# Optimization experiments

Measured on AMD Instinct MI355X. Metric: run time of the kernel, lower is better.

Reference implementation:

```python
import jax, jax.numpy as jnp
import numpy as np

N_MID = 100000
D = 64
B = 64
S = 256
K = 10
BIG_NEG = -2.0**32 + 1.0


def _din(q, facts, mask, W1, b1, W2, b2, W3, b3):
    # q broadcastable to facts shape; facts [..., T, D]; mask [..., T]
    qb = jnp.broadcast_to(q, facts.shape)
    x = jnp.concatenate([qb, facts, qb - facts, qb * facts], axis=-1)  # [..., T, 4D]
    h = jax.nn.sigmoid(x @ W1 + b1)
    h = jax.nn.sigmoid(h @ W2 + b2)
    s = (h @ W3 + b3)[..., 0]  # [..., T]
    s = jnp.where(mask == 1.0, s, BIG_NEG)
    a = jax.nn.softmax(s, axis=-1)
    return jnp.einsum('...t,...td->...d', a, facts)


def _prelu(x, alpha):
    return jnp.maximum(x, 0.0) + alpha * jnp.minimum(x, 0.0)


def setup_inputs():
    key = jax.random.key(0)
    ks = iter(jax.random.split(key, 48))
    def nrm(shape, scale=0.05):
        return jax.random.normal(next(ks), shape, dtype=jnp.float32) * scale
    inp = {}
    inp['mid'] = jax.random.randint(next(ks), (B,), 0, N_MID)
    inp['click_his'] = jax.random.randint(next(ks), (B, S), 0, N_MID)
    inp['unclick_his'] = jax.random.randint(next(ks), (B, K * S), 0, N_MID)
    inp['click_mask'] = jnp.ones((B, S), jnp.float32)
    inp['unclick_mask'] = jnp.ones((B, K * S), jnp.float32)
    inp['emb'] = nrm((N_MID, D), 0.1)
    for p in ('s', 'c', 'u'):  # search / click / unclick attention MLPs
        inp[p + 'W1'] = nrm((4 * D, 80)); inp[p + 'b1'] = jnp.zeros((80,), jnp.float32)
        inp[p + 'W2'] = nrm((80, 40));    inp[p + 'b2'] = jnp.zeros((40,), jnp.float32)
        inp[p + 'W3'] = nrm((40, 1));     inp[p + 'b3'] = jnp.zeros((1,), jnp.float32)
    F = 3 * D
    inp['bn_g'] = jnp.ones((F,), jnp.float32); inp['bn_b'] = jnp.zeros((F,), jnp.float32)
    inp['bn_m'] = jnp.zeros((F,), jnp.float32); inp['bn_v'] = jnp.ones((F,), jnp.float32)
    inp['fW1'] = nrm((F, 200)); inp['fb1'] = jnp.zeros((200,), jnp.float32); inp['a1'] = 0.25 * jnp.ones((200,), jnp.float32)
    inp['fW2'] = nrm((200, 80)); inp['fb2'] = jnp.zeros((80,), jnp.float32); inp['a2'] = 0.25 * jnp.ones((80,), jnp.float32)
    inp['fW3'] = nrm((80, 2)); inp['fb3'] = jnp.zeros((2,), jnp.float32)
    return inp


def reference(mid, click_his, unclick_his, click_mask, unclick_mask, emb,
              sW1, sb1, sW2, sb2, sW3, sb3,
              cW1, cb1, cW2, cb2, cW3, cb3,
              uW1, ub1, uW2, ub2, uW3, ub3,
              bn_g, bn_b, bn_m, bn_v,
              fW1, fb1, a1, fW2, fb2, a2, fW3, fb3):
    item = emb[mid]                                        # [B, D]
    click = emb[click_his] * click_mask[..., None]         # [B, S, D]
    unclick = emb[unclick_his] * unclick_mask[..., None]   # [B, K*S, D]
    uf = unclick.reshape(B, S, K, D)
    umask = unclick_mask.reshape(B, S, K)
    # din_attention_1: per clicked item, attend over its K unclicked items
    un_att = _din(click[:, :, None, :], uf, umask, sW1, sb1, sW2, sb2, sW3, sb3)  # [B, S, D]
    # denoise: project unclick rep onto click rep (shared component)
    dot = jnp.sum(un_att * click, axis=-1, keepdims=True)
    nrm2 = jnp.sum(click * click, axis=-1, keepdims=True) + 1e-12  # ||target||^2
    shared = dot * click / nrm2
    att1 = _din(item[:, None, :], click + shared, click_mask, cW1, cb1, cW2, cb2, cW3, cb3)  # [B, D]
    att2 = _din(item[:, None, :], un_att, click_mask, uW1, ub1, uW2, ub2, uW3, ub3)          # [B, D]
    x = jnp.concatenate([item, att1, att2], axis=-1)  # [B, 3D]
    x = (x - bn_m) / jnp.sqrt(bn_v + 1e-3) * bn_g + bn_b  # inference batchnorm
    x = _prelu(x @ fW1 + fb1, a1)
    x = _prelu(x @ fW2 + fb2, a2)
    logits = x @ fW3 + fb3
    return jax.nn.softmax(logits, axis=-1) + 1e-8
```

## Files before the change

kernel.cpp:

```cpp
#include <hip/hip_runtime.h>
#include <hip/hip_bf16.h>
#include <math.h>

#define BB 64
#define SS 256
#define KK 10
#define DD 64
#define FF 192
#define FH1 200
#define FH2 80
#define BIG_NEG_F (-4294967295.0f)

#define XSTR 200
#define H1STR 104

#define W1ELTS (80 * XSTR)
#define W2ELTS (48 * H1STR)
#define WREG   (W1ELTS + W2ELTS)

typedef __bf16 bfrag __attribute__((ext_vector_type(8)));
typedef float f32x4 __attribute__((ext_vector_type(4)));

__device__ __forceinline__ float sigm_(float x) { return 1.0f / (1.0f + __expf(-x)); }

__global__ __launch_bounds__(256) void k_prep(
    const float* __restrict__ sW1, const float* __restrict__ sW2,
    const float* __restrict__ cW1, const float* __restrict__ cW2,
    const float* __restrict__ uW1, const float* __restrict__ uW2,
    __bf16* __restrict__ Wt)
{
    const int p = blockIdx.x, g = blockIdx.y;
    const float* W1 = (p == 0) ? sW1 : (p == 1) ? cW1 : uW1;
    const float* W2 = (p == 0) ? sW2 : (p == 1) ? cW2 : uW2;
    __bf16* o1 = Wt + p * WREG;
    __bf16* o2 = o1 + W1ELTS;
    for (int e = g * 256 + threadIdx.x; e < W1ELTS; e += 2560) {
        const int n = e / XSTR, k = e % XSTR;
        float v = 0.0f;
        if (k < 64)       v = W1[k * 80 + n] + W1[(128 + k) * 80 + n];
        else if (k < 128) { const int kk = k - 64;  v = W1[(64 + kk) * 80 + n] - W1[(128 + kk) * 80 + n]; }
        else if (k < 192) { const int kk = k - 128; v = W1[(192 + kk) * 80 + n]; }
        o1[e] = (__bf16)v;
    }
    for (int e = g * 256 + threadIdx.x; e < W2ELTS; e += 2560) {
        const int n = e / H1STR, k = e % H1STR;
        o2[e] = (__bf16)((n < 40 && k < 80) ? W2[k * 40 + n] : 0.0f);
    }
}

__device__ __forceinline__ void mlp_core(
    const float* qv, const float* fv,
    const __bf16* __restrict__ sW1, __bf16* __restrict__ sH1w,
    const bfrag* wb2, const float* b1v, const float* b2v, const float* w3v,
    int quad, int l15, float* score)
{
    bfrag af[6];
    #pragma unroll
    for (int j = 0; j < 8; ++j) {
        af[0][j] = (__bf16)qv[j];
        af[1][j] = (__bf16)qv[8 + j];
        af[2][j] = (__bf16)fv[j];
        af[3][j] = (__bf16)fv[8 + j];
        af[4][j] = (__bf16)(qv[j] * fv[j]);
        af[5][j] = (__bf16)(qv[8 + j] * fv[8 + j]);
    }

    f32x4 acc[5];
    #pragma unroll
    for (int nt = 0; nt < 5; ++nt) acc[nt] = (f32x4){0.f, 0.f, 0.f, 0.f};
    {
        const __bf16* wbase = sW1 + l15 * XSTR + quad * 8;
        #pragma unroll
        for (int nt = 0; nt < 5; ++nt) {
            const __bf16* wp = wbase + nt * 16 * XSTR;
            #pragma unroll
            for (int kc = 0; kc < 6; ++kc)
                acc[nt] = __builtin_amdgcn_mfma_f32_16x16x32_bf16(
                    af[kc], *(const bfrag*)(wp + kc * 32), acc[nt], 0, 0, 0);
        }
    }

    #pragma unroll
    for (int nt = 0; nt < 5; ++nt) {
        #pragma unroll
        for (int rg = 0; rg < 4; ++rg)
            sH1w[(quad * 4 + rg) * H1STR + nt * 16 + l15] =
                (__bf16)sigm_(acc[nt][rg] + b1v[nt]);
    }
    #pragma unroll
    for (int rg = 0; rg < 4; ++rg)
        sH1w[(quad * 4 + rg) * H1STR + 80 + l15] = (__bf16)0.0f;

    bfrag af2[3];
    {
        const __bf16* hrow = sH1w + l15 * H1STR + quad * 8;
        #pragma unroll
        for (int kc = 0; kc < 3; ++kc) af2[kc] = *(const bfrag*)(hrow + kc * 32);
    }
    f32x4 acc2[3];
    #pragma unroll
    for (int nt = 0; nt < 3; ++nt) acc2[nt] = (f32x4){0.f, 0.f, 0.f, 0.f};
    #pragma unroll
    for (int nt = 0; nt < 3; ++nt)
        #pragma unroll
        for (int kc = 0; kc < 3; ++kc)
            acc2[nt] = __builtin_amdgcn_mfma_f32_16x16x32_bf16(
                af2[kc], wb2[nt * 3 + kc], acc2[nt], 0, 0, 0);

    float part[4] = {0.f, 0.f, 0.f, 0.f};
    #pragma unroll
    for (int nt = 0; nt < 3; ++nt) {
        #pragma unroll
        for (int rg = 0; rg < 4; ++rg)
            part[rg] += sigm_(acc2[nt][rg] + b2v[nt]) * w3v[nt];
    }
    #pragma unroll
    for (int off = 1; off < 16; off <<= 1) {
        #pragma unroll
        for (int rg = 0; rg < 4; ++rg)
            part[rg] += __shfl_xor(part[rg], off, 64);
    }
    #pragma unroll
    for (int rg = 0; rg < 4; ++rg) score[rg] = part[rg];
}

__global__ __launch_bounds__(320) void k_din0(
    const int* __restrict__ click_his, const int* __restrict__ unclick_his,
    const float* __restrict__ click_mask, const float* __restrict__ unclick_mask,
    const float* __restrict__ emb, const __bf16* __restrict__ Wt,
    const float* __restrict__ b1, const float* __restrict__ b2,
    const float* __restrict__ W3, const float* __restrict__ b3,
    float* __restrict__ unatt, float* __restrict__ coef)
{
    __shared__ __align__(16) __bf16 sW1[80 * XSTR];
    __shared__ __align__(16) __bf16 sH1[5 * 16 * H1STR];
    __shared__ float ssc[80];

    const int t = threadIdx.x;
    const int wave = t >> 6, lane = t & 63;
    const int quad = lane >> 4, l15 = lane & 15;

    {
        const uint4* s1 = (const uint4*)Wt;
        uint4* d1 = (uint4*)sW1;
        for (int e = t; e < W1ELTS / 8; e += 320) d1[e] = s1[e];
    }

    bfrag wb2[9];
    float b1v[5], b2v[3], w3v[3];
    {
        const __bf16* w2g = Wt + W1ELTS;
        #pragma unroll
        for (int nt = 0; nt < 3; ++nt)
            #pragma unroll
            for (int kc = 0; kc < 3; ++kc)
                wb2[nt * 3 + kc] = *(const bfrag*)(w2g + (nt * 16 + l15) * H1STR + kc * 32 + quad * 8);
        #pragma unroll
        for (int nt = 0; nt < 5; ++nt) b1v[nt] = b1[nt * 16 + l15];
        #pragma unroll
        for (int nt = 0; nt < 3; ++nt) {
            const int n = nt * 16 + l15;
            b2v[nt] = (n < 40) ? b2[n] : 0.0f;
            w3v[nt] = (n < 40) ? W3[n] : 0.0f;
        }
    }
    const float b3v = b3[0];

    const int row = 16 * wave + l15;
    const int m   = blockIdx.x * 80 + row;
    const int bs  = blockIdx.x * 8 + row / 10;
    float qv[16], fv[16];
    {
        const float* qp = emb + (size_t)click_his[bs] * DD;
        const float* fp = emb + (size_t)unclick_his[m] * DD;
        const float qs = click_mask[bs], fs = unclick_mask[m];
        const int c = quad * 8;
        *(float4*)(qv + 0)  = *(const float4*)(qp + c);
        *(float4*)(qv + 4)  = *(const float4*)(qp + c + 4);
        *(float4*)(qv + 8)  = *(const float4*)(qp + 32 + c);
        *(float4*)(qv + 12) = *(const float4*)(qp + 32 + c + 4);
        *(float4*)(fv + 0)  = *(const float4*)(fp + c);
        *(float4*)(fv + 4)  = *(const float4*)(fp + c + 4);
        *(float4*)(fv + 8)  = *(const float4*)(fp + 32 + c);
        *(float4*)(fv + 12) = *(const float4*)(fp + 32 + c + 4);
        #pragma unroll
        for (int i = 0; i < 16; ++i) { qv[i] *= qs; fv[i] *= fs; }
    }

    float fpre[2][KK], qpre[2];
    #pragma unroll
    for (int jj = 0; jj < 2; ++jj) {
        const int j = wave + 5 * jj;
        if (j < 8) {
            const int bsj = blockIdx.x * 8 + j;
            #pragma unroll
            for (int k = 0; k < KK; ++k) {
                const int off = bsj * KK + k;
                fpre[jj][k] = emb[(size_t)unclick_his[off] * DD + lane] * unclick_mask[off];
            }
            qpre[jj] = emb[(size_t)click_his[bsj] * DD + lane] * click_mask[bsj];
        }
    }
    __syncthreads();

    float score[4];
    mlp_core(qv, fv, sW1, sH1 + wave * 16 * H1STR, wb2, b1v, b2v, w3v, quad, l15, score);

    if (l15 == 0) {
        #pragma unroll
        for (int rg = 0; rg < 4; ++rg) {
            const int r2 = 16 * wave + quad * 4 + rg;
            const int m2 = blockIdx.x * 80 + r2;
            ssc[r2] = (unclick_mask[m2] == 1.0f) ? (score[rg] + b3v) : BIG_NEG_F;
        }
    }
    __syncthreads();

    #pragma unroll
    for (int jj = 0; jj < 2; ++jj) {
        const int j = wave + 5 * jj;
        if (j >= 8) continue;
        const int bsj = blockIdx.x * 8 + j;
        float a[KK];
        float mx = -INFINITY;
        #pragma unroll
        for (int k = 0; k < KK; ++k) { a[k] = ssc[j * KK + k]; mx = fmaxf(mx, a[k]); }
        float sum = 0.0f;
        #pragma unroll
        for (int k = 0; k < KK; ++k) { a[k] = __expf(a[k] - mx); sum += a[k]; }
        const float inv = 1.0f / sum;
        float acc3 = 0.0f;
        #pragma unroll
        for (int k = 0; k < KK; ++k) acc3 += a[k] * fpre[jj][k];
        acc3 *= inv;
        unatt[(size_t)bsj * DD + lane] = acc3;
        const float qv2 = qpre[jj];
        float dp = acc3 * qv2, nq = qv2 * qv2;
        #pragma unroll
        for (int o = 32; o > 0; o >>= 1) {
            dp += __shfl_down(dp, o, 64);
            nq += __shfl_down(nq, o, 64);
        }
        if (lane == 0) coef[bsj] = 1.0f + dp / (nq + 1e-12f);
    }
}

__global__ __launch_bounds__(128) void k_din12(
    const int* __restrict__ mid, const int* __restrict__ click_his,
    const float* __restrict__ click_mask,
    const float* __restrict__ emb, const float* __restrict__ unatt,
    const float* __restrict__ coef, const __bf16* __restrict__ Wt,
    const float* __restrict__ cb1, const float* __restrict__ cb2,
    const float* __restrict__ cW3, const float* __restrict__ cb3,
    const float* __restrict__ ub1, const float* __restrict__ ub2,
    const float* __restrict__ uW3, const float* __restrict__ ub3,
    float* __restrict__ scores_c, float* __restrict__ scores_u)
{
    __shared__ __align__(16) __bf16 sW1[80 * XSTR];
    __shared__ __align__(16) __bf16 sH1[2 * 16 * H1STR];

    const int t = threadIdx.x;
    const int mode = blockIdx.y;
    const int wave = t >> 6, lane = t & 63;
    const int quad = lane >> 4, l15 = lane & 15;

    const float* b1 = mode ? ub1 : cb1;
    const float* b2 = mode ? ub2 : cb2;
    const float* W3 = mode ? uW3 : cW3;
    const float* b3 = mode ? ub3 : cb3;
    const __bf16* wreg = Wt + (mode + 1) * WREG;

    {
        const uint4* s1 = (const uint4*)wreg;
        uint4* d1 = (uint4*)sW1;
        for (int e = t; e < W1ELTS / 8; e += 128) d1[e] = s1[e];
    }

    bfrag wb2[9];
    float b1v[5], b2v[3], w3v[3];
    {
        const __bf16* w2g = wreg + W1ELTS;
        #pragma unroll
        for (int nt = 0; nt < 3; ++nt)
            #pragma unroll
            for (int kc = 0; kc < 3; ++kc)
                wb2[nt * 3 + kc] = *(const bfrag*)(w2g + (nt * 16 + l15) * H1STR + kc * 32 + quad * 8);
        #pragma unroll
        for (int nt = 0; nt < 5; ++nt) b1v[nt] = b1[nt * 16 + l15];
        #pragma unroll
        for (int nt = 0; nt < 3; ++nt) {
            const int n = nt * 16 + l15;
            b2v[nt] = (n < 40) ? b2[n] : 0.0f;
            w3v[nt] = (n < 40) ? W3[n] : 0.0f;
        }
    }
    const float b3v = b3[0];

    const int row = 16 * wave + l15;
    const int m   = blockIdx.x * 32 + row;
    const int b   = m >> 8;
    float qv[16], fv[16];
    {
        const float* qp = emb + (size_t)mid[b] * DD;
        const float* fp; float fs;
        if (mode == 0) { fp = emb + (size_t)click_his[m] * DD; fs = click_mask[m] * coef[m]; }
        else           { fp = unatt + (size_t)m * DD; fs = 1.0f; }
        const int c = quad * 8;
        *(float4*)(qv + 0)  = *(const float4*)(qp + c);
        *(float4*)(qv + 4)  = *(const float4*)(qp + c + 4);
        *(float4*)(qv + 8)  = *(const float4*)(qp + 32 + c);
        *(float4*)(qv + 12) = *(const float4*)(qp + 32 + c + 4);
        *(float4*)(fv + 0)  = *(const float4*)(fp + c);
        *(float4*)(fv + 4)  = *(const float4*)(fp + c + 4);
        *(float4*)(fv + 8)  = *(const float4*)(fp + 32 + c);
        *(float4*)(fv + 12) = *(const float4*)(fp + 32 + c + 4);
        #pragma unroll
        for (int i = 0; i < 16; ++i) fv[i] *= fs;
    }
    __syncthreads();

    float score[4];
    mlp_core(qv, fv, sW1, sH1 + wave * 16 * H1STR, wb2, b1v, b2v, w3v, quad, l15, score);

    if (l15 == 0) {
        float* dst = mode ? scores_u : scores_c;
        #pragma unroll
        for (int rg = 0; rg < 4; ++rg) {
            const int m2 = blockIdx.x * 32 + 16 * wave + quad * 4 + rg;
            dst[m2] = (click_mask[m2] == 1.0f) ? (score[rg] + b3v) : BIG_NEG_F;
        }
    }
}

__global__ __launch_bounds__(1024) void k_tail(
    const int* __restrict__ mid, const int* __restrict__ click_his,
    const float* __restrict__ click_mask,
    const float* __restrict__ emb, const float* __restrict__ unatt,
    const float* __restrict__ coef,
    const float* __restrict__ scores_c, const float* __restrict__ scores_u,
    const float* __restrict__ bn_g, const float* __restrict__ bn_b,
    const float* __restrict__ bn_m, const float* __restrict__ bn_v,
    const float* __restrict__ fW1, const float* __restrict__ fb1, const float* __restrict__ a1,
    const float* __restrict__ fW2, const float* __restrict__ fb2, const float* __restrict__ a2,
    const float* __restrict__ fW3, const float* __restrict__ fb3,
    float* __restrict__ out)
{
    const int b = blockIdx.x, t = threadIdx.x;
    const int wave = t >> 6, lane = t & 63;
    const int ty = wave >> 3, w8 = wave & 7;
    const int s0 = w8 * 32;

    __shared__ float sa[2][SS];
    __shared__ float smax[16], ssum[16];
    __shared__ float part[16][72];
    __shared__ float x[FF];
    __shared__ float ph1[4][FH1];
    __shared__ float h1s[FH1];
    __shared__ float ph2[8][FH2];
    __shared__ float h2s[FH2];
    __shared__ float red2[2];

    if (t < DD) x[t] = emb[(size_t)mid[b] * DD + t];

    const float* scp = ty ? scores_u : scores_c;
    const float sc = (lane < 32) ? scp[b * SS + s0 + lane] : -INFINITY;
    float mloc = sc;
    #pragma unroll
    for (int o = 32; o > 0; o >>= 1) mloc = fmaxf(mloc, __shfl_xor(mloc, o, 64));
    if (lane == 0) smax[wave] = mloc;
    __syncthreads();

    float mt = smax[ty * 8];
    #pragma unroll
    for (int i = 1; i < 8; ++i) mt = fmaxf(mt, smax[ty * 8 + i]);
    const float e = (lane < 32) ? __expf(sc - mt) : 0.0f;
    if (lane < 32) sa[ty][s0 + lane] = e;
    float sloc = e;
    #pragma unroll
    for (int o = 32; o > 0; o >>= 1) sloc += __shfl_xor(sloc, o, 64);
    if (lane == 0) ssum[wave] = sloc;
    __syncthreads();

    float den = 0.0f;
    #pragma unroll
    for (int i = 0; i < 8; ++i) den += ssum[ty * 8 + i];
    const float inv = 1.0f / den;

    float acc = 0.0f;
    #pragma unroll 8
    for (int i = 0; i < 32; ++i) {
        const int s2 = s0 + i;
        const int bs = b * SS + s2;
        const float fv = ty ? unatt[(size_t)bs * DD + lane]
                            : emb[(size_t)click_his[bs] * DD + lane] * click_mask[bs] * coef[bs];
        acc += sa[ty][s2] * fv;
    }
    part[wave][lane] = acc * inv;
    __syncthreads();

    if (t < 128) {
        const int tt = t >> 6, d = t & 63;
        float v = 0.0f;
        #pragma unroll
        for (int i = 0; i < 8; ++i) v += part[tt * 8 + i][d];
        x[DD + tt * DD + d] = v;
    }
    __syncthreads();

    if (t < FF) x[t] = (x[t] - bn_m[t]) * rsqrtf(bn_v[t] + 1e-3f) * bn_g[t] + bn_b[t];
    __syncthreads();

    if (t < 800) {
        const int n = t % FH1, c = t / FH1;
        float p = 0.0f;
        #pragma unroll 8
        for (int i = c * 48; i < c * 48 + 48; ++i) p += x[i] * fW1[i * FH1 + n];
        ph1[c][n] = p;
    }
    __syncthreads();
    if (t < FH1) {
        const float a = ph1[0][t] + ph1[1][t] + ph1[2][t] + ph1[3][t] + fb1[t];
        h1s[t] = fmaxf(a, 0.0f) + a1[t] * fminf(a, 0.0f);
    }
    __syncthreads();

    if (t < 640) {
        const int n = t % FH2, c = t / FH2;
        float p = 0.0f;
        #pragma unroll 5
        for (int i = c * 25; i < c * 25 + 25; ++i) p += h1s[i] * fW2[i * FH2 + n];
        ph2[c][n] = p;
    }
    __syncthreads();
    if (t < FH2) {
        float a = fb2[t];
        #pragma unroll
        for (int c = 0; c < 8; ++c) a += ph2[c][t];
        h2s[t] = fmaxf(a, 0.0f) + a2[t] * fminf(a, 0.0f);
    }
    __syncthreads();

    if (t < 128) {
        const int o = t >> 6;
        float p = h2s[lane] * fW3[lane * 2 + o];
        if (lane < 16) p += h2s[64 + lane] * fW3[(64 + lane) * 2 + o];
        #pragma unroll
        for (int off = 32; off > 0; off >>= 1) p += __shfl_down(p, off, 64);
        if (lane == 0) red2[o] = p + fb3[o];
    }
    __syncthreads();
    if (t == 0) {
        const float l0 = red2[0], l1 = red2[1];
        const float mx = fmaxf(l0, l1);
        const float e0 = __expf(l0 - mx), e1 = __expf(l1 - mx);
        const float invs = 1.0f / (e0 + e1);
        out[b * 2 + 0] = e0 * invs + 1e-8f;
        out[b * 2 + 1] = e1 * invs + 1e-8f;
    }
}

extern "C" void kernel_launch(void* const* d_in, const int* in_sizes, int n_in,
                              void* d_out, int out_size, void* d_ws, size_t ws_size,
                              hipStream_t stream) {
    const int*   mid          = (const int*)d_in[0];
    const int*   click_his    = (const int*)d_in[1];
    const int*   unclick_his  = (const int*)d_in[2];
    const float* click_mask   = (const float*)d_in[3];
    const float* unclick_mask = (const float*)d_in[4];
    const float* emb          = (const float*)d_in[5];
    const float* sW1 = (const float*)d_in[6];  const float* sb1 = (const float*)d_in[7];
    const float* sW2 = (const float*)d_in[8];  const float* sb2 = (const float*)d_in[9];
    const float* sW3 = (const float*)d_in[10]; const float* sb3 = (const float*)d_in[11];
    const float* cW1 = (const float*)d_in[12]; const float* cb1 = (const float*)d_in[13];
    const float* cW2 = (const float*)d_in[14]; const float* cb2 = (const float*)d_in[15];
    const float* cW3 = (const float*)d_in[16]; const float* cb3 = (const float*)d_in[17];
    const float* uW1 = (const float*)d_in[18]; const float* ub1 = (const float*)d_in[19];
    const float* uW2 = (const float*)d_in[20]; const float* ub2 = (const float*)d_in[21];
    const float* uW3 = (const float*)d_in[22]; const float* ub3 = (const float*)d_in[23];
    const float* bn_g = (const float*)d_in[24]; const float* bn_b = (const float*)d_in[25];
    const float* bn_m = (const float*)d_in[26]; const float* bn_v = (const float*)d_in[27];
    const float* fW1 = (const float*)d_in[28]; const float* fb1 = (const float*)d_in[29];
    const float* a1  = (const float*)d_in[30];
    const float* fW2 = (const float*)d_in[31]; const float* fb2 = (const float*)d_in[32];
    const float* a2  = (const float*)d_in[33];
    const float* fW3 = (const float*)d_in[34]; const float* fb3 = (const float*)d_in[35];

    float* out = (float*)d_out;

    char* w = (char*)d_ws;
    __bf16* Wt      = (__bf16*)(w + 0);
    float* scores_c = (float*)(w + 125952);
    float* scores_u = (float*)(w + 191488);
    float* coef     = (float*)(w + 257024);
    float* unatt    = (float*)(w + 322560);

    hipLaunchKernelGGL(k_prep, dim3(3, 10), dim3(256), 0, stream,
        sW1, sW2, cW1, cW2, uW1, uW2, Wt);

    hipLaunchKernelGGL(k_din0, dim3(2048), dim3(320), 0, stream,
        click_his, unclick_his, click_mask, unclick_mask, emb, Wt,
        sb1, sb2, sW3, sb3, unatt, coef);

    hipLaunchKernelGGL(k_din12, dim3(512, 2), dim3(128), 0, stream,
        mid, click_his, click_mask, emb, unatt, coef, Wt,
        cb1, cb2, cW3, cb3, ub1, ub2, uW3, ub3, scores_c, scores_u);

    hipLaunchKernelGGL(k_tail, dim3(BB), dim3(1024), 0, stream,
        mid, click_his, click_mask, emb, unatt, coef, scores_c, scores_u,
        bn_g, bn_b, bn_m, bn_v, fW1, fb1, a1, fW2, fb2, a2, fW3, fb3, out);
}
```

Measured before the change: 246.1 us.

## Amortize shared weight staging over more rows per block with prefetched gathers

k_din0 now gives each wave 80 rows (5 MFMA tiles, 8 click items) and loops over them, prefetching the next tile's embedding gathers while the current tile runs the MLP. Blocks drop from 2048 to 512, so the 32KB W1 copy into LDS is paid a quarter as often. k_din12 doubles rows per block to amortize the same staging, and k_prep now reads W1 coalesced while writing transposed. The cost is fewer blocks in flight and more registers for the double-buffered row data, which may reduce parallelism for the latency-bound gathers.

```diff
diff --git a/kernel.cpp b/kernel.cpp
--- a/kernel.cpp
+++ b/kernel.cpp
@@ -34,13 +34,14 @@
     const float* W2 = (p == 0) ? sW2 : (p == 1) ? cW2 : uW2;
     __bf16* o1 = Wt + p * WREG;
     __bf16* o2 = o1 + W1ELTS;
-    for (int e = g * 256 + threadIdx.x; e < W1ELTS; e += 2560) {
-        const int n = e / XSTR, k = e % XSTR;
-        float v = 0.0f;
-        if (k < 64)       v = W1[k * 80 + n] + W1[(128 + k) * 80 + n];
-        else if (k < 128) { const int kk = k - 64;  v = W1[(64 + kk) * 80 + n] - W1[(128 + kk) * 80 + n]; }
-        else if (k < 192) { const int kk = k - 128; v = W1[(192 + kk) * 80 + n]; }
-        o1[e] = (__bf16)v;
+    for (int e = g * 256 + threadIdx.x; e < 200 * 80; e += 2560) {
+        const int k = e / 80, n = e % 80;
+        float v;
+        if (k < 64)       v = W1[k * 80 + n] + W1[(k + 128) * 80 + n];
+        else if (k < 128) v = W1[k * 80 + n] - W1[(k + 64) * 80 + n];
+        else if (k < 192) v = W1[(k + 64) * 80 + n];
+        else              v = 0.0f;
+        o1[n * XSTR + k] = (__bf16)v;
     }
     for (int e = g * 256 + threadIdx.x; e < W2ELTS; e += 2560) {
         const int n = e / H1STR, k = e % H1STR;
@@ -124,7 +125,7 @@
     for (int rg = 0; rg < 4; ++rg) score[rg] = part[rg];
 }
 
-__global__ __launch_bounds__(320) void k_din0(
+__global__ __launch_bounds__(256) void k_din0(
     const int* __restrict__ click_his, const int* __restrict__ unclick_his,
     const float* __restrict__ click_mask, const float* __restrict__ unclick_mask,
     const float* __restrict__ emb, const __bf16* __restrict__ Wt,
@@ -133,8 +134,8 @@
     float* __restrict__ unatt, float* __restrict__ coef)
 {
     __shared__ __align__(16) __bf16 sW1[80 * XSTR];
-    __shared__ __align__(16) __bf16 sH1[5 * 16 * H1STR];
-    __shared__ float ssc[80];
+    __shared__ __align__(16) __bf16 sH1[4][16 * H1STR];
+    __shared__ float ssc[4][80];
 
     const int t = threadIdx.x;
     const int wave = t >> 6, lane = t & 63;
@@ -143,7 +144,7 @@
     {
         const uint4* s1 = (const uint4*)Wt;
         uint4* d1 = (uint4*)sW1;
-        for (int e = t; e < W1ELTS / 8; e += 320) d1[e] = s1[e];
+        for (int e = t; e < W1ELTS / 8; e += 256) d1[e] = s1[e];
     }
 
     bfrag wb2[9];
@@ -166,15 +167,15 @@
     }
     const float b3v = b3[0];
 
-    const int row = 16 * wave + l15;
-    const int m   = blockIdx.x * 80 + row;
-    const int bs  = blockIdx.x * 8 + row / 10;
-    float qv[16], fv[16];
-    {
+    const int wbase = (blockIdx.x * 4 + wave) * 80;
+    const int c = quad * 8;
+
+    auto gload = [&](int tt, float* qv, float* fv) {
+        const int m  = wbase + tt * 16 + l15;
+        const int bs = m / 10;
         const float* qp = emb + (size_t)click_his[bs] * DD;
         const float* fp = emb + (size_t)unclick_his[m] * DD;
         const float qs = click_mask[bs], fs = unclick_mask[m];
-        const int c = quad * 8;
         *(float4*)(qv + 0)  = *(const float4*)(qp + c);
         *(float4*)(qv + 4)  = *(const float4*)(qp + c + 4);
         *(float4*)(qv + 8)  = *(const float4*)(qp + 32 + c);
@@ -185,56 +186,56 @@
         *(float4*)(fv + 12) = *(const float4*)(fp + 32 + c + 4);
         #pragma unroll
         for (int i = 0; i < 16; ++i) { qv[i] *= qs; fv[i] *= fs; }
-    }
-
-    float fpre[2][KK], qpre[2];
-    #pragma unroll
-    for (int jj = 0; jj < 2; ++jj) {
-        const int j = wave + 5 * jj;
-        if (j < 8) {
-            const int bsj = blockIdx.x * 8 + j;
+    };
+
+    float qv[2][16], fv[2][16];
+    gload(0, qv[0], fv[0]);
+    __syncthreads();
+
+    for (int tt = 0; tt < 5; ++tt) {
+        if (tt < 4) gload(tt + 1, qv[(tt + 1) & 1], fv[(tt + 1) & 1]);
+        float score[4];
+        mlp_core(qv[tt & 1], fv[tt & 1], sW1, sH1[wave], wb2, b1v, b2v, w3v, quad, l15, score);
+        if (l15 == 0) {
             #pragma unroll
-            for (int k = 0; k < KK; ++k) {
-                const int off = bsj * KK + k;
-                fpre[jj][k] = emb[(size_t)unclick_his[off] * DD + lane] * unclick_mask[off];
+            for (int rg = 0; rg < 4; ++rg) {
+                const int r2 = tt * 16 + quad * 4 + rg;
+                const int m2 = wbase + r2;
+                ssc[wave][r2] = (unclick_mask[m2] == 1.0f) ? (score[rg] + b3v) : BIG_NEG_F;
             }
-            qpre[jj] = emb[(size_t)click_his[bsj] * DD + lane] * click_mask[bsj];
-        }
-    }
-    __syncthreads();
-
-    float score[4];
-    mlp_core(qv, fv, sW1, sH1 + wave * 16 * H1STR, wb2, b1v, b2v, w3v, quad, l15, score);
-
-    if (l15 == 0) {
-        #pragma unroll
-        for (int rg = 0; rg < 4; ++rg) {
-            const int r2 = 16 * wave + quad * 4 + rg;
-            const int m2 = blockIdx.x * 80 + r2;
-            ssc[r2] = (unclick_mask[m2] == 1.0f) ? (score[rg] + b3v) : BIG_NEG_F;
-        }
-    }
-    __syncthreads();
-
-    #pragma unroll
-    for (int jj = 0; jj < 2; ++jj) {
-        const int j = wave + 5 * jj;
-        if (j >= 8) continue;
-        const int bsj = blockIdx.x * 8 + j;
+        }
+    }
+    __syncthreads();
+
+    float fr[2][KK], qr[2];
+    auto kload = [&](int j) {
+        const int bsj = blockIdx.x * 32 + wave * 8 + j;
+        const int jj = j & 1;
+        #pragma unroll
+        for (int k = 0; k < KK; ++k) {
+            const int off = bsj * KK + k;
+            fr[jj][k] = emb[(size_t)unclick_his[off] * DD + lane] * unclick_mask[off];
+        }
+        qr[jj] = emb[(size_t)click_his[bsj] * DD + lane] * click_mask[bsj];
+    };
+    kload(0);
+    for (int j = 0; j < 8; ++j) {
+        if (j < 7) kload(j + 1);
+        const int bsj = blockIdx.x * 32 + wave * 8 + j;
         float a[KK];
         float mx = -INFINITY;
         #pragma unroll
-        for (int k = 0; k < KK; ++k) { a[k] = ssc[j * KK + k]; mx = fmaxf(mx, a[k]); }
+        for (int k = 0; k < KK; ++k) { a[k] = ssc[wave][j * KK + k]; mx = fmaxf(mx, a[k]); }
         float sum = 0.0f;
         #pragma unroll
         for (int k = 0; k < KK; ++k) { a[k] = __expf(a[k] - mx); sum += a[k]; }
         const float inv = 1.0f / sum;
         float acc3 = 0.0f;
         #pragma unroll
-        for (int k = 0; k < KK; ++k) acc3 += a[k] * fpre[jj][k];
+        for (int k = 0; k < KK; ++k) acc3 += a[k] * fr[j & 1][k];
         acc3 *= inv;
         unatt[(size_t)bsj * DD + lane] = acc3;
-        const float qv2 = qpre[jj];
+        const float qv2 = qr[j & 1];
         float dp = acc3 * qv2, nq = qv2 * qv2;
         #pragma unroll
         for (int o = 32; o > 0; o >>= 1) {
@@ -245,7 +246,7 @@
     }
 }
 
-__global__ __launch_bounds__(128) void k_din12(
+__global__ __launch_bounds__(256) void k_din12(
     const int* __restrict__ mid, const int* __restrict__ click_his,
     const float* __restrict__ click_mask,
     const float* __restrict__ emb, const float* __restrict__ unatt,
@@ -257,7 +258,7 @@
     float* __restrict__ scores_c, float* __restrict__ scores_u)
 {
     __shared__ __align__(16) __bf16 sW1[80 * XSTR];
-    __shared__ __align__(16) __bf16 sH1[2 * 16 * H1STR];
+    __shared__ __align__(16) __bf16 sH1[4][16 * H1STR];
 
     const int t = threadIdx.x;
     const int mode = blockIdx.y;
@@ -273,7 +274,7 @@
     {
         const uint4* s1 = (const uint4*)wreg;
         uint4* d1 = (uint4*)sW1;
-        for (int e = t; e < W1ELTS / 8; e += 128) d1[e] = s1[e];
+        for (int e = t; e < W1ELTS / 8; e += 256) d1[e] = s1[e];
     }
 
     bfrag wb2[9];
@@ -297,7 +298,7 @@
     const float b3v = b3[0];
 
     const int row = 16 * wave + l15;
-    const int m   = blockIdx.x * 32 + row;
+    const int m   = blockIdx.x * 64 + row;
     const int b   = m >> 8;
     float qv[16], fv[16];
     {
@@ -320,13 +321,13 @@
     __syncthreads();
 
     float score[4];
-    mlp_core(qv, fv, sW1, sH1 + wave * 16 * H1STR, wb2, b1v, b2v, w3v, quad, l15, score);
+    mlp_core(qv, fv, sW1, sH1[wave], wb2, b1v, b2v, w3v, quad, l15, score);
 
     if (l15 == 0) {
         float* dst = mode ? scores_u : scores_c;
         #pragma unroll
         for (int rg = 0; rg < 4; ++rg) {
-            const int m2 = blockIdx.x * 32 + 16 * wave + quad * 4 + rg;
+            const int m2 = blockIdx.x * 64 + 16 * wave + quad * 4 + rg;
             dst[m2] = (click_mask[m2] == 1.0f) ? (score[rg] + b3v) : BIG_NEG_F;
         }
     }
@@ -411,11 +412,11 @@
     __syncthreads();
 
     if (t < 800) {
-        const int n = t % FH1, c = t / FH1;
+        const int n = t % FH1, cc = t / FH1;
         float p = 0.0f;
         #pragma unroll 8
-        for (int i = c * 48; i < c * 48 + 48; ++i) p += x[i] * fW1[i * FH1 + n];
-        ph1[c][n] = p;
+        for (int i = cc * 48; i < cc * 48 + 48; ++i) p += x[i] * fW1[i * FH1 + n];
+        ph1[cc][n] = p;
     }
     __syncthreads();
     if (t < FH1) {
@@ -425,17 +426,17 @@
     __syncthreads();
 
     if (t < 640) {
-        const int n = t % FH2, c = t / FH2;
+        const int n = t % FH2, cc = t / FH2;
         float p = 0.0f;
         #pragma unroll 5
-        for (int i = c * 25; i < c * 25 + 25; ++i) p += h1s[i] * fW2[i * FH2 + n];
-        ph2[c][n] = p;
+        for (int i = cc * 25; i < cc * 25 + 25; ++i) p += h1s[i] * fW2[i * FH2 + n];
+        ph2[cc][n] = p;
     }
     __syncthreads();
     if (t < FH2) {
         float a = fb2[t];
         #pragma unroll
-        for (int c = 0; c < 8; ++c) a += ph2[c][t];
+        for (int cc = 0; cc < 8; ++cc) a += ph2[cc][t];
         h2s[t] = fmaxf(a, 0.0f) + a2[t] * fminf(a, 0.0f);
     }
     __syncthreads();
@@ -497,11 +498,11 @@
     hipLaunchKernelGGL(k_prep, dim3(3, 10), dim3(256), 0, stream,
         sW1, sW2, cW1, cW2, uW1, uW2, Wt);
 
-    hipLaunchKernelGGL(k_din0, dim3(2048), dim3(320), 0, stream,
+    hipLaunchKernelGGL(k_din0, dim3(512), dim3(256), 0, stream,
         click_his, unclick_his, click_mask, unclick_mask, emb, Wt,
         sb1, sb2, sW3, sb3, unatt, coef);
 
-    hipLaunchKernelGGL(k_din12, dim3(512, 2), dim3(128), 0, stream,
+    hipLaunchKernelGGL(k_din12, dim3(256, 2), dim3(256), 0, stream,
         mid, click_his, click_mask, emb, unatt, coef, Wt,
         cb1, cb2, cW3, cb3, ub1, ub2, uW3, ub3, scores_c, scores_u);
 
```

New measurement: 261.0 us. 1.06x slower.

## Enlarge din12 blocks, defer din0 gathers, coalesce prep weight transpose

Applied to the files above, without the earlier changes.

k_din12 now runs 512-thread blocks over 128 rows each instead of 128-thread blocks over 32 rows, so each staged copy of the bf16 W1 tile in shared memory is reused by four times as many rows. In k_din0, the per-lane embedding gathers used for the weighted sum are moved out of registers held across the MLP and issued after the softmax, which lowers register pressure. k_prep now iterates in source order, giving coalesced reads and scattered transposed writes. The trade-offs are fewer, larger blocks in din12 and gather latency now exposed after the score reduction in din0.

```diff
diff --git a/kernel.cpp b/kernel.cpp
--- a/kernel.cpp
+++ b/kernel.cpp
@@ -34,13 +34,14 @@
     const float* W2 = (p == 0) ? sW2 : (p == 1) ? cW2 : uW2;
     __bf16* o1 = Wt + p * WREG;
     __bf16* o2 = o1 + W1ELTS;
-    for (int e = g * 256 + threadIdx.x; e < W1ELTS; e += 2560) {
-        const int n = e / XSTR, k = e % XSTR;
-        float v = 0.0f;
-        if (k < 64)       v = W1[k * 80 + n] + W1[(128 + k) * 80 + n];
-        else if (k < 128) { const int kk = k - 64;  v = W1[(64 + kk) * 80 + n] - W1[(128 + kk) * 80 + n]; }
-        else if (k < 192) { const int kk = k - 128; v = W1[(192 + kk) * 80 + n]; }
-        o1[e] = (__bf16)v;
+    for (int e = g * 256 + threadIdx.x; e < 200 * 80; e += 2560) {
+        const int k = e / 80, n = e % 80;
+        float v;
+        if (k < 64)       v = W1[k * 80 + n] + W1[(k + 128) * 80 + n];
+        else if (k < 128) v = W1[k * 80 + n] - W1[(k + 64) * 80 + n];
+        else if (k < 192) v = W1[(k + 64) * 80 + n];
+        else              v = 0.0f;
+        o1[n * XSTR + k] = (__bf16)v;
     }
     for (int e = g * 256 + threadIdx.x; e < W2ELTS; e += 2560) {
         const int n = e / H1STR, k = e % H1STR;
@@ -186,21 +187,6 @@
         #pragma unroll
         for (int i = 0; i < 16; ++i) { qv[i] *= qs; fv[i] *= fs; }
     }
-
-    float fpre[2][KK], qpre[2];
-    #pragma unroll
-    for (int jj = 0; jj < 2; ++jj) {
-        const int j = wave + 5 * jj;
-        if (j < 8) {
-            const int bsj = blockIdx.x * 8 + j;
-            #pragma unroll
-            for (int k = 0; k < KK; ++k) {
-                const int off = bsj * KK + k;
-                fpre[jj][k] = emb[(size_t)unclick_his[off] * DD + lane] * unclick_mask[off];
-            }
-            qpre[jj] = emb[(size_t)click_his[bsj] * DD + lane] * click_mask[bsj];
-        }
-    }
     __syncthreads();
 
     float score[4];
@@ -216,10 +202,7 @@
     }
     __syncthreads();
 
-    #pragma unroll
-    for (int jj = 0; jj < 2; ++jj) {
-        const int j = wave + 5 * jj;
-        if (j >= 8) continue;
+    for (int j = wave; j < 8; j += 5) {
         const int bsj = blockIdx.x * 8 + j;
         float a[KK];
         float mx = -INFINITY;
@@ -231,10 +214,13 @@
         const float inv = 1.0f / sum;
         float acc3 = 0.0f;
         #pragma unroll
-        for (int k = 0; k < KK; ++k) acc3 += a[k] * fpre[jj][k];
+        for (int k = 0; k < KK; ++k) {
+            const int off = bsj * KK + k;
+            acc3 += a[k] * (emb[(size_t)unclick_his[off] * DD + lane] * unclick_mask[off]);
+        }
         acc3 *= inv;
         unatt[(size_t)bsj * DD + lane] = acc3;
-        const float qv2 = qpre[jj];
+        const float qv2 = emb[(size_t)click_his[bsj] * DD + lane] * click_mask[bsj];
         float dp = acc3 * qv2, nq = qv2 * qv2;
         #pragma unroll
         for (int o = 32; o > 0; o >>= 1) {
@@ -245,7 +231,7 @@
     }
 }
 
-__global__ __launch_bounds__(128) void k_din12(
+__global__ __launch_bounds__(512) void k_din12(
     const int* __restrict__ mid, const int* __restrict__ click_his,
     const float* __restrict__ click_mask,
     const float* __restrict__ emb, const float* __restrict__ unatt,
@@ -257,7 +243,7 @@
     float* __restrict__ scores_c, float* __restrict__ scores_u)
 {
     __shared__ __align__(16) __bf16 sW1[80 * XSTR];
-    __shared__ __align__(16) __bf16 sH1[2 * 16 * H1STR];
+    __shared__ __align__(16) __bf16 sH1[8][16 * H1STR];
 
     const int t = threadIdx.x;
     const int mode = blockIdx.y;
@@ -273,7 +259,7 @@
     {
         const uint4* s1 = (const uint4*)wreg;
         uint4* d1 = (uint4*)sW1;
-        for (int e = t; e < W1ELTS / 8; e += 128) d1[e] = s1[e];
+        for (int e = t; e < W1ELTS / 8; e += 512) d1[e] = s1[e];
     }
 
     bfrag wb2[9];
@@ -297,7 +283,7 @@
     const float b3v = b3[0];
 
     const int row = 16 * wave + l15;
-    const int m   = blockIdx.x * 32 + row;
+    const int m   = blockIdx.x * 128 + row;
     const int b   = m >> 8;
     float qv[16], fv[16];
     {
@@ -320,13 +306,13 @@
     __syncthreads();
 
     float score[4];
-    mlp_core(qv, fv, sW1, sH1 + wave * 16 * H1STR, wb2, b1v, b2v, w3v, quad, l15, score);
+    mlp_core(qv, fv, sW1, sH1[wave], wb2, b1v, b2v, w3v, quad, l15, score);
 
     if (l15 == 0) {
         float* dst = mode ? scores_u : scores_c;
         #pragma unroll
         for (int rg = 0; rg < 4; ++rg) {
-            const int m2 = blockIdx.x * 32 + 16 * wave + quad * 4 + rg;
+            const int m2 = blockIdx.x * 128 + 16 * wave + quad * 4 + rg;
             dst[m2] = (click_mask[m2] == 1.0f) ? (score[rg] + b3v) : BIG_NEG_F;
         }
     }
@@ -411,11 +397,11 @@
     __syncthreads();
 
     if (t < 800) {
-        const int n = t % FH1, c = t / FH1;
+        const int n = t % FH1, cc = t / FH1;
         float p = 0.0f;
         #pragma unroll 8
-        for (int i = c * 48; i < c * 48 + 48; ++i) p += x[i] * fW1[i * FH1 + n];
-        ph1[c][n] = p;
+        for (int i = cc * 48; i < cc * 48 + 48; ++i) p += x[i] * fW1[i * FH1 + n];
+        ph1[cc][n] = p;
     }
     __syncthreads();
     if (t < FH1) {
@@ -425,17 +411,17 @@
     __syncthreads();
 
     if (t < 640) {
-        const int n = t % FH2, c = t / FH2;
+        const int n = t % FH2, cc = t / FH2;
         float p = 0.0f;
         #pragma unroll 5
-        for (int i = c * 25; i < c * 25 + 25; ++i) p += h1s[i] * fW2[i * FH2 + n];
-        ph2[c][n] = p;
+        for (int i = cc * 25; i < cc * 25 + 25; ++i) p += h1s[i] * fW2[i * FH2 + n];
+        ph2[cc][n] = p;
     }
     __syncthreads();
     if (t < FH2) {
         float a = fb2[t];
         #pragma unroll
-        for (int c = 0; c < 8; ++c) a += ph2[c][t];
+        for (int cc = 0; cc < 8; ++cc) a += ph2[cc][t];
         h2s[t] = fmaxf(a, 0.0f) + a2[t] * fminf(a, 0.0f);
     }
     __syncthreads();
@@ -501,7 +487,7 @@
         click_his, unclick_his, click_mask, unclick_mask, emb, Wt,
         sb1, sb2, sW3, sb3, unatt, coef);
 
-    hipLaunchKernelGGL(k_din12, dim3(512, 2), dim3(128), 0, stream,
+    hipLaunchKernelGGL(k_din12, dim3(128, 2), dim3(512), 0, stream,
         mid, click_his, click_mask, emb, unatt, coef, Wt,
         cb1, cb2, cW3, cb3, ub1, ub2, uW3, ub3, scores_c, scores_u);
 
```

After: 222.5 us. 9.6% less time.
